# Optimization experiments

Hardware: AMD Instinct MI355X
Metric: run time of the kernel (lower is better)

The kernel has to match this reference:

```python
import jax, jax.numpy as jnp
import numpy as np

BN_EPS = 1e-5
NN_EPS = 1e-8

def _bn_relu(h, gamma, beta):
    # training-mode BatchNorm1d over (B, L) per channel, biased variance
    mean = jnp.mean(h, axis=(0, 2), keepdims=True)
    var = jnp.mean((h - mean) ** 2, axis=(0, 2), keepdims=True)
    hn = (h - mean) * jax.lax.rsqrt(var + BN_EPS)
    return jax.nn.relu(hn * gamma[None, :, None] + beta[None, :, None])

def setup_inputs() -> dict:
    key = jax.random.key(0)
    ks = jax.random.split(key, 8)
    B, N, M, Cin, Cout = 2, 2048, 8192, 512, 256
    return {
        "x1": jax.random.normal(ks[0], (B, N, Cin), jnp.float32),
        "p1": jax.random.uniform(ks[1], (B, N, 3), jnp.float32),
        "x2": jax.random.normal(ks[2], (B, M, Cout), jnp.float32),
        "p2": jax.random.uniform(ks[3], (B, M, 3), jnp.float32),
        "W_up": jax.random.normal(ks[4], (Cout, Cin), jnp.float32) * (1.0 / np.sqrt(Cin)),
        "gamma_up": jnp.ones((Cout,), jnp.float32),
        "beta_up": jnp.zeros((Cout,), jnp.float32),
        "W_lat": jax.random.normal(ks[5], (Cout, Cout), jnp.float32) * (1.0 / np.sqrt(Cout)),
        "gamma_lat": jnp.ones((Cout,), jnp.float32),
        "beta_lat": jnp.zeros((Cout,), jnp.float32),
    }

def reference(x1, p1, x2, p2, W_up, gamma_up, beta_up, W_lat, gamma_lat, beta_lat):
    B, M, _ = p2.shape
    # up_mlp: 1x1 conv (bias=False) + BN + ReLU -> (B, Cout, N)
    h1 = _bn_relu(jnp.einsum('bnc,oc->bon', x1, W_up), gamma_up, beta_up)
    # three_nn: squared distances from each p2 query to all p1 points
    d2 = (jnp.sum(p2 ** 2, -1)[:, :, None] + jnp.sum(p1 ** 2, -1)[:, None, :]
          - 2.0 * jnp.einsum('bmd,bnd->bmn', p2, p1))  # (B, M, N)
    neg_d, idx = jax.lax.top_k(-d2, 3)                 # 3 smallest squared dists
    dist = -neg_d                                      # (B, M, 3)
    dist_recip = 1.0 / (dist + NN_EPS)
    weight = dist_recip / jnp.sum(dist_recip, axis=2, keepdims=True)  # (B, M, 3)
    # three_interpolate: weighted gather of h1 along point axis
    C = h1.shape[1]
    g = jnp.take_along_axis(h1, idx.reshape(B, 1, M * 3), axis=2).reshape(B, C, M, 3)
    interp = jnp.einsum('bcmk,bmk->bcm', g, weight)    # (B, Cout, M)
    # lateral_mlp on x2
    h2 = _bn_relu(jnp.einsum('bmc,oc->bom', x2, W_lat), gamma_lat, beta_lat)
    y = interp + h2                                    # (B, Cout, M)
    return jnp.transpose(y, (0, 2, 1)), p2             # (B, M, Cout), (B, M, 3)
```

## Files before the change

### kernel.cpp

```cpp
#include <hip/hip_runtime.h>

#define BATCH 2
#define NPTS  2048
#define MPTS  8192
#define CIN1  512
#define CIN2  256
#define COUT  256
#define ROWS1 (BATCH*NPTS)
#define ROWS2 (BATCH*MPTS)
#define BN_EPS 1e-5f
#define NN_EPS 1e-8f

#define NCHUNK 16
#define CHUNK  (NPTS / NCHUNK)

typedef __attribute__((ext_vector_type(8))) short  bf16x8;
typedef __attribute__((ext_vector_type(4))) float  f32x4;

#define AS1 __attribute__((address_space(1)))
#define AS3 __attribute__((address_space(3)))

__device__ __forceinline__ unsigned short bf16_rne(float x) {
    unsigned u = __float_as_uint(x);
    u += 0x7FFFu + ((u >> 16) & 1u);
    return (unsigned short)(u >> 16);
}
__device__ __forceinline__ float bf16_f32(unsigned short h) {
    return __uint_as_float(((unsigned)h) << 16);
}

__device__ __forceinline__ void gload16(const void* g, void* l) {
    __builtin_amdgcn_global_load_lds((const AS1 unsigned int*)g,
                                     (AS3 unsigned int*)l, 16, 0, 0);
}

__global__ __launch_bounds__(256)
void split_pre(const float* __restrict__ x1, const float* __restrict__ x2,
               const float* __restrict__ wu, const float* __restrict__ wl,
               unsigned short* __restrict__ x1h, unsigned short* __restrict__ x1l,
               unsigned short* __restrict__ x2h, unsigned short* __restrict__ x2l,
               unsigned short* __restrict__ wuh, unsigned short* __restrict__ wul,
               unsigned short* __restrict__ wlh, unsigned short* __restrict__ wll) {
    const int bid = blockIdx.x;
    const float* src; unsigned short *dh, *dl; int K, tile;
    if (bid < 1024)      { src = x1; dh = x1h; dl = x1l; K = CIN1; tile = bid; }
    else if (bid < 3072) { src = x2; dh = x2h; dl = x2l; K = CIN2; tile = bid - 1024; }
    else if (bid < 3136) { src = wu; dh = wuh; dl = wul; K = CIN1; tile = bid - 3072; }
    else                 { src = wl; dh = wlh; dl = wll; K = CIN2; tile = bid - 3136; }
    const int ktiles = K / 32;
    const int rt = tile / ktiles, kt = tile - rt * ktiles;
    const int t = threadIdx.x, row = t >> 2, lg = t & 3;

    const float* s = src + (size_t)(rt * 64 + row) * K + kt * 32 + lg * 8;
    const float4 v0 = *(const float4*)s;
    const float4 v1 = *(const float4*)(s + 4);
    const float vv[8] = {v0.x, v0.y, v0.z, v0.w, v1.x, v1.y, v1.z, v1.w};
    bf16x8 h, l;
    #pragma unroll
    for (int i = 0; i < 8; ++i) {
        const unsigned short hh = bf16_rne(vv[i]);
        h[i] = (short)hh;
        l[i] = (short)bf16_rne(vv[i] - bf16_f32(hh));
    }
    const unsigned off = ((unsigned)(row * 64 + lg * 16)) ^ ((unsigned)((row & 7) << 4));
    *(bf16x8*)((char*)dh + (size_t)tile * 4096 + off) = h;
    *(bf16x8*)((char*)dl + (size_t)tile * 4096 + off) = l;
}

template<int KTILES, int KSPLIT, bool FUSE_STATS>
__global__ __launch_bounds__(256)
void gemm_pre(const unsigned short* __restrict__ Ah_img, const unsigned short* __restrict__ Al_img,
              const unsigned short* __restrict__ Bh_img, const unsigned short* __restrict__ Bl_img,
              float* __restrict__ C, float* __restrict__ stats) {
    constexpr int KT = KTILES / KSPLIT;
    __shared__ __align__(16) unsigned char lds[2][4][4096];
    __shared__ float red[64][8];

    const int tid = threadIdx.x;
    const int lane = tid & 63, wid = tid >> 6;
    const int m0 = blockIdx.y * 64, o0 = blockIdx.x * 64;
    const int kt0 = blockIdx.z * KT;
    const int wy = wid >> 1, wx = wid & 1;
    const int lr = lane & 15, lg = lane >> 4;

    const unsigned short* src;
    size_t base;
    switch (wid) {
        case 0:  src = Ah_img; base = ((size_t)blockIdx.y * KTILES + kt0) * 2048; break;
        case 1:  src = Al_img; base = ((size_t)blockIdx.y * KTILES + kt0) * 2048; break;
        case 2:  src = Bh_img; base = ((size_t)blockIdx.x * KTILES + kt0) * 2048; break;
        default: src = Bl_img; base = ((size_t)blockIdx.x * KTILES + kt0) * 2048; break;
    }

    f32x4 acc[2][2];
    #pragma unroll
    for (int i = 0; i < 2; ++i)
        #pragma unroll
        for (int j = 0; j < 2; ++j)
            acc[i][j] = (f32x4){0.f, 0.f, 0.f, 0.f};

    auto STAGE = [&](int buf, int t) {
        const unsigned short* s = src + base + (size_t)t * 2048;
        char* l = (char*)&lds[buf][wid][0];
        #pragma unroll
        for (int c = 0; c < 4; ++c)
            gload16(s + c * 512 + lane * 8, l + c * 1024);
    };

    auto FOFF = [&](int row) -> int {
        return (row * 64 + lg * 16) ^ ((row & 7) << 4);
    };

    STAGE(0, 0);
    asm volatile("s_waitcnt vmcnt(0)" ::: "memory");
    __builtin_amdgcn_s_barrier();
    __builtin_amdgcn_sched_barrier(0);

    int cur = 0;
    for (int t = 0; t < KT; ++t) {
        if (t + 1 < KT) STAGE(cur ^ 1, t + 1);

        const char* LAh = (const char*)&lds[cur][0][0];
        const char* LAl = (const char*)&lds[cur][1][0];
        const char* LBh = (const char*)&lds[cur][2][0];
        const char* LBl = (const char*)&lds[cur][3][0];

        bf16x8 fah[2], fal[2], fbh[2], fbl[2];
        #pragma unroll
        for (int i = 0; i < 2; ++i) {
            const int off = FOFF(wy * 32 + i * 16 + lr);
            fah[i] = *(const bf16x8*)(LAh + off);
            fal[i] = *(const bf16x8*)(LAl + off);
        }
        #pragma unroll
        for (int j = 0; j < 2; ++j) {
            const int off = FOFF(wx * 32 + j * 16 + lr);
            fbh[j] = *(const bf16x8*)(LBh + off);
            fbl[j] = *(const bf16x8*)(LBl + off);
        }
        #pragma unroll
        for (int i = 0; i < 2; ++i)
            #pragma unroll
            for (int j = 0; j < 2; ++j) {
                acc[i][j] = __builtin_amdgcn_mfma_f32_16x16x32_bf16(fah[i], fbh[j], acc[i][j], 0, 0, 0);
                acc[i][j] = __builtin_amdgcn_mfma_f32_16x16x32_bf16(fal[i], fbh[j], acc[i][j], 0, 0, 0);
                acc[i][j] = __builtin_amdgcn_mfma_f32_16x16x32_bf16(fah[i], fbl[j], acc[i][j], 0, 0, 0);
            }

        asm volatile("s_waitcnt vmcnt(0)" ::: "memory");
        __builtin_amdgcn_s_barrier();
        __builtin_amdgcn_sched_barrier(0);
        cur ^= 1;
    }

    #pragma unroll
    for (int i = 0; i < 2; ++i)
        #pragma unroll
        for (int j = 0; j < 2; ++j) {
            const int col = o0 + wx * 32 + j * 16 + lr;
            const int rbase = m0 + wy * 32 + i * 16 + lg * 4;
            #pragma unroll
            for (int r = 0; r < 4; ++r) {
                if (KSPLIT > 1)
                    atomicAdd(&C[(size_t)(rbase + r) * COUT + col], acc[i][j][r]);
                else
                    C[(size_t)(rbase + r) * COUT + col] = acc[i][j][r];
            }
        }

    if constexpr (FUSE_STATS) {
        #pragma unroll
        for (int j = 0; j < 2; ++j) {
            float s = 0.f;
            #pragma unroll
            for (int i = 0; i < 2; ++i)
                #pragma unroll
                for (int r = 0; r < 4; ++r)
                    s += acc[i][j][r];
            red[wx * 32 + j * 16 + lr][wy * 4 + lg] = s;
        }
        __syncthreads();
        if (tid < 64) {
            float s = 0.f;
            #pragma unroll
            for (int k = 0; k < 8; ++k) s += red[tid][k];
            atomicAdd(&stats[o0 + tid], s);
        }
        __syncthreads();
        #pragma unroll
        for (int j = 0; j < 2; ++j) {
            float q = 0.f;
            #pragma unroll
            for (int i = 0; i < 2; ++i)
                #pragma unroll
                for (int r = 0; r < 4; ++r)
                    q = fmaf(acc[i][j][r], acc[i][j][r], q);
            red[wx * 32 + j * 16 + lr][wy * 4 + lg] = q;
        }
        __syncthreads();
        if (tid < 64) {
            float q = 0.f;
            #pragma unroll
            for (int k = 0; k < 8; ++k) q += red[tid][k];
            atomicAdd(&stats[COUT + o0 + tid], q);
        }
    }
}

__global__ __launch_bounds__(256)
void colsum256(const float* __restrict__ X, int rowsPerBlock,
               float* __restrict__ out) {
    const int c = threadIdx.x;
    const int r0 = blockIdx.x * rowsPerBlock;
    float s = 0.f, q = 0.f;
    for (int r = 0; r < rowsPerBlock; ++r) {
        float v = X[(size_t)(r0 + r) * COUT + c];
        s += v;
        q = fmaf(v, v, q);
    }
    atomicAdd(&out[c], s);
    atomicAdd(&out[COUT + c], q);
}

__global__ __launch_bounds__(256)
void three_nn_part(const float* __restrict__ p1, const float* __restrict__ p2,
                   float2* __restrict__ part) {
    __shared__ float4 pts[CHUNK];
    const int b = blockIdx.z;
    const int c = blockIdx.y;
    const int t = threadIdx.x;
    const int n0 = c * CHUNK;
    if (t < CHUNK) {
        const float* P1 = p1 + ((size_t)b * NPTS + n0) * 3;
        float x = P1[t * 3 + 0], y = P1[t * 3 + 1], z = P1[t * 3 + 2];
        pts[t] = make_float4(x, y, z, x * x + y * y + z * z);
    }
    __syncthreads();
    const int m = blockIdx.x * 256 + t;
    const float* q = p2 + ((size_t)b * MPTS + m) * 3;
    const float qx = q[0], qy = q[1], qz = q[2];
    const float s2 = qx * qx + qy * qy + qz * qz;
    float d0 = 1e30f, d1 = 1e30f, d2 = 1e30f;
    int   i0 = 0,     i1 = 0,     i2 = 0;
    #pragma unroll 4
    for (int n = 0; n < CHUNK; ++n) {
        float4 p = pts[n];
        float dot = p.x * qx + p.y * qy + p.z * qz;
        float d = s2 + p.w - 2.0f * dot;
        if (d < d2) {
            if (d < d1) {
                d2 = d1; i2 = i1;
                if (d < d0) { d1 = d0; i1 = i0; d0 = d; i0 = n0 + n; }
                else        { d1 = d;  i1 = n0 + n; }
            } else { d2 = d; i2 = n0 + n; }
        }
    }
    float2* o = part + ((size_t)(b * MPTS + m) * NCHUNK + c) * 3;
    o[0] = make_float2(d0, __int_as_float(i0));
    o[1] = make_float2(d1, __int_as_float(i1));
    o[2] = make_float2(d2, __int_as_float(i2));
}

__global__ __launch_bounds__(256)
void final_combine(const float* __restrict__ h1, const float* __restrict__ stats,
                   const float* __restrict__ g1, const float* __restrict__ b1,
                   const float* __restrict__ g2, const float* __restrict__ b2,
                   const float2* __restrict__ part, float* __restrict__ out) {
    const int t = threadIdx.x;
    const int row = blockIdx.x * 4 + (t >> 6);
    const int c = (t & 63) * 4;
    const int b = row >> 13;

    float d0 = 1e30f, d1 = 1e30f, d2 = 1e30f;
    int   i0 = 0,     i1 = 0,     i2 = 0;
    {
        const float4* pp = (const float4*)(part + (size_t)row * NCHUNK * 3);
        #pragma unroll
        for (int j = 0; j < NCHUNK * 3 / 2; ++j) {
            float4 v = pp[j];
            #pragma unroll
            for (int h = 0; h < 2; ++h) {
                float d = h ? v.z : v.x;
                int   i = __float_as_int(h ? v.w : v.y);
                if (d < d2) {
                    if (d < d1) {
                        d2 = d1; i2 = i1;
                        if (d < d0) { d1 = d0; i1 = i0; d0 = d; i0 = i; }
                        else        { d1 = d;  i1 = i; }
                    } else { d2 = d; i2 = i; }
                }
            }
        }
    }
    const float r0 = 1.0f / (d0 + NN_EPS);
    const float r1 = 1.0f / (d1 + NN_EPS);
    const float r2 = 1.0f / (d2 + NN_EPS);
    const float irs = 1.0f / (r0 + r1 + r2);
    const float w0 = r0 * irs, w1 = r1 * irs, w2 = r2 * irs;

    const float4 sum1 = *(const float4*)&stats[c];
    const float4 sq1  = *(const float4*)&stats[COUT + c];
    const float4 sum2 = *(const float4*)&stats[512 + c];
    const float4 sq2  = *(const float4*)&stats[768 + c];
    const float4 gg1  = *(const float4*)&g1[c];
    const float4 bb1  = *(const float4*)&b1[c];
    const float4 gg2  = *(const float4*)&g2[c];
    const float4 bb2  = *(const float4*)&b2[c];

    const float inv1 = 1.0f / (float)ROWS1, inv2 = 1.0f / (float)ROWS2;
    float4 sc1, sh1, sc2, sh2;
    {
        float m, v;
        m = sum1.x*inv1; v = fmaf(-m,m,sq1.x*inv1); sc1.x = gg1.x/sqrtf(v+BN_EPS); sh1.x = fmaf(-m,sc1.x,bb1.x);
        m = sum1.y*inv1; v = fmaf(-m,m,sq1.y*inv1); sc1.y = gg1.y/sqrtf(v+BN_EPS); sh1.y = fmaf(-m,sc1.y,bb1.y);
        m = sum1.z*inv1; v = fmaf(-m,m,sq1.z*inv1); sc1.z = gg1.z/sqrtf(v+BN_EPS); sh1.z = fmaf(-m,sc1.z,bb1.z);
        m = sum1.w*inv1; v = fmaf(-m,m,sq1.w*inv1); sc1.w = gg1.w/sqrtf(v+BN_EPS); sh1.w = fmaf(-m,sc1.w,bb1.w);
        m = sum2.x*inv2; v = fmaf(-m,m,sq2.x*inv2); sc2.x = gg2.x/sqrtf(v+BN_EPS); sh2.x = fmaf(-m,sc2.x,bb2.x);
        m = sum2.y*inv2; v = fmaf(-m,m,sq2.y*inv2); sc2.y = gg2.y/sqrtf(v+BN_EPS); sh2.y = fmaf(-m,sc2.y,bb2.y);
        m = sum2.z*inv2; v = fmaf(-m,m,sq2.z*inv2); sc2.z = gg2.z/sqrtf(v+BN_EPS); sh2.z = fmaf(-m,sc2.z,bb2.z);
        m = sum2.w*inv2; v = fmaf(-m,m,sq2.w*inv2); sc2.w = gg2.w/sqrtf(v+BN_EPS); sh2.w = fmaf(-m,sc2.w,bb2.w);
    }

    const float* hb = h1 + (size_t)b * NPTS * COUT + c;
    const float4 h0 = *(const float4*)(hb + (size_t)i0 * COUT);
    const float4 h4 = *(const float4*)(hb + (size_t)i1 * COUT);
    const float4 h8 = *(const float4*)(hb + (size_t)i2 * COUT);

    const size_t oi = (size_t)row * COUT + c;
    float4 yv = *(const float4*)&out[oi];
    float4 r;
    r.x = fmaxf(fmaf(yv.x, sc2.x, sh2.x), 0.f)
        + w0 * fmaxf(fmaf(h0.x, sc1.x, sh1.x), 0.f)
        + w1 * fmaxf(fmaf(h4.x, sc1.x, sh1.x), 0.f)
        + w2 * fmaxf(fmaf(h8.x, sc1.x, sh1.x), 0.f);
    r.y = fmaxf(fmaf(yv.y, sc2.y, sh2.y), 0.f)
        + w0 * fmaxf(fmaf(h0.y, sc1.y, sh1.y), 0.f)
        + w1 * fmaxf(fmaf(h4.y, sc1.y, sh1.y), 0.f)
        + w2 * fmaxf(fmaf(h8.y, sc1.y, sh1.y), 0.f);
    r.z = fmaxf(fmaf(yv.z, sc2.z, sh2.z), 0.f)
        + w0 * fmaxf(fmaf(h0.z, sc1.z, sh1.z), 0.f)
        + w1 * fmaxf(fmaf(h4.z, sc1.z, sh1.z), 0.f)
        + w2 * fmaxf(fmaf(h8.z, sc1.z, sh1.z), 0.f);
    r.w = fmaxf(fmaf(yv.w, sc2.w, sh2.w), 0.f)
        + w0 * fmaxf(fmaf(h0.w, sc1.w, sh1.w), 0.f)
        + w1 * fmaxf(fmaf(h4.w, sc1.w, sh1.w), 0.f)
        + w2 * fmaxf(fmaf(h8.w, sc1.w, sh1.w), 0.f);
    *(float4*)&out[oi] = r;
}

extern "C" void kernel_launch(void* const* d_in, const int* in_sizes, int n_in,
                              void* d_out, int out_size, void* d_ws, size_t ws_size,
                              hipStream_t stream) {
    const float* x1       = (const float*)d_in[0];
    const float* p1       = (const float*)d_in[1];
    const float* x2       = (const float*)d_in[2];
    const float* p2       = (const float*)d_in[3];
    const float* W_up     = (const float*)d_in[4];
    const float* gamma_up = (const float*)d_in[5];
    const float* beta_up  = (const float*)d_in[6];
    const float* W_lat    = (const float*)d_in[7];
    const float* gamma_lat= (const float*)d_in[8];
    const float* beta_lat = (const float*)d_in[9];
    float* out = (float*)d_out;

    char* w = (char*)d_ws;
    unsigned short* x1h = (unsigned short*)(w);
    unsigned short* x1l = (unsigned short*)(w + (4u<<20));
    unsigned short* x2h = (unsigned short*)(w + (8u<<20));
    unsigned short* x2l = (unsigned short*)(w + (16u<<20));
    unsigned short* wuh = (unsigned short*)(w + (24u<<20));
    unsigned short* wul = (unsigned short*)(w + (24u<<20) + (256u<<10));
    unsigned short* wlh = (unsigned short*)(w + (24u<<20) + (512u<<10));
    unsigned short* wll = (unsigned short*)(w + (24u<<20) + (640u<<10));
    float*  h1    = (float*)(w + (25u<<20));
    float*  stats = (float*)(w + (29u<<20));
    float2* part  = (float2*)(w + (29u<<20) + (16u<<10));

    hipMemsetAsync(stats, 0, 1024 * sizeof(float), stream);
    hipMemsetAsync(h1, 0, (size_t)ROWS1 * COUT * sizeof(float), stream);

    split_pre<<<3168, 256, 0, stream>>>(x1, x2, W_up, W_lat,
                                        x1h, x1l, x2h, x2l, wuh, wul, wlh, wll);

    gemm_pre<CIN1/32, 4, false><<<dim3(COUT/64, ROWS1/64, 4), 256, 0, stream>>>(
        x1h, x1l, wuh, wul, h1, nullptr);
    colsum256<<<256, 256, 0, stream>>>(h1, ROWS1 / 256, stats);

    gemm_pre<CIN2/32, 1, true><<<dim3(COUT/64, ROWS2/64, 1), 256, 0, stream>>>(
        x2h, x2l, wlh, wll, out, stats + 512);

    three_nn_part<<<dim3(MPTS / 256, NCHUNK, BATCH), 256, 0, stream>>>(p1, p2, part);

    final_combine<<<ROWS2 / 4, 256, 0, stream>>>(h1, stats, gamma_up, beta_up,
                                                 gamma_lat, beta_lat, part, out);

    hipMemcpyAsync(out + (size_t)ROWS2 * COUT, p2,
                   (size_t)ROWS2 * 3 * sizeof(float),
                   hipMemcpyDeviceToDevice, stream);
}
```

Baseline: 194.7 us.

## Merge prep with three_nn, merge both GEMMs, triple-buffer LDS pipeline

The bf16 split preprocessing and the three-NN partial search now share one launch, with block-index ranges selecting the work. Both projection GEMMs are merged into a single launch so the two independent workloads fill the GPU together. The GEMM K-loop moves from double to triple buffering with a partial vmcnt wait, so loads stay two stages ahead. The two memsets become one contiguous memset covering h1 and stats. This cuts launch count and tail idle time, but raises LDS per block, which may lower occupancy.

Result: no change. 192.2 us (-1.3%).

```diff
diff --git a/kernel.cpp b/kernel.cpp
--- a/kernel.cpp
+++ b/kernel.cpp
@@ -28,68 +28,111 @@
 __device__ __forceinline__ float bf16_f32(unsigned short h) {
     return __uint_as_float(((unsigned)h) << 16);
 }
-
 __device__ __forceinline__ void gload16(const void* g, void* l) {
     __builtin_amdgcn_global_load_lds((const AS1 unsigned int*)g,
                                      (AS3 unsigned int*)l, 16, 0, 0);
 }
 
 __global__ __launch_bounds__(256)
-void split_pre(const float* __restrict__ x1, const float* __restrict__ x2,
-               const float* __restrict__ wu, const float* __restrict__ wl,
-               unsigned short* __restrict__ x1h, unsigned short* __restrict__ x1l,
-               unsigned short* __restrict__ x2h, unsigned short* __restrict__ x2l,
-               unsigned short* __restrict__ wuh, unsigned short* __restrict__ wul,
-               unsigned short* __restrict__ wlh, unsigned short* __restrict__ wll) {
+void prep_fused(const float* __restrict__ x1, const float* __restrict__ x2,
+                const float* __restrict__ wu, const float* __restrict__ wl,
+                const float* __restrict__ p1, const float* __restrict__ p2,
+                unsigned short* __restrict__ x1h, unsigned short* __restrict__ x1l,
+                unsigned short* __restrict__ x2h, unsigned short* __restrict__ x2l,
+                unsigned short* __restrict__ wuh, unsigned short* __restrict__ wul,
+                unsigned short* __restrict__ wlh, unsigned short* __restrict__ wll,
+                float2* __restrict__ part) {
     const int bid = blockIdx.x;
-    const float* src; unsigned short *dh, *dl; int K, tile;
-    if (bid < 1024)      { src = x1; dh = x1h; dl = x1l; K = CIN1; tile = bid; }
-    else if (bid < 3072) { src = x2; dh = x2h; dl = x2l; K = CIN2; tile = bid - 1024; }
-    else if (bid < 3136) { src = wu; dh = wuh; dl = wul; K = CIN1; tile = bid - 3072; }
-    else                 { src = wl; dh = wlh; dl = wll; K = CIN2; tile = bid - 3136; }
-    const int ktiles = K / 32;
-    const int rt = tile / ktiles, kt = tile - rt * ktiles;
-    const int t = threadIdx.x, row = t >> 2, lg = t & 3;
-
-    const float* s = src + (size_t)(rt * 64 + row) * K + kt * 32 + lg * 8;
-    const float4 v0 = *(const float4*)s;
-    const float4 v1 = *(const float4*)(s + 4);
-    const float vv[8] = {v0.x, v0.y, v0.z, v0.w, v1.x, v1.y, v1.z, v1.w};
-    bf16x8 h, l;
-    #pragma unroll
-    for (int i = 0; i < 8; ++i) {
-        const unsigned short hh = bf16_rne(vv[i]);
-        h[i] = (short)hh;
-        l[i] = (short)bf16_rne(vv[i] - bf16_f32(hh));
-    }
-    const unsigned off = ((unsigned)(row * 64 + lg * 16)) ^ ((unsigned)((row & 7) << 4));
-    *(bf16x8*)((char*)dh + (size_t)tile * 4096 + off) = h;
-    *(bf16x8*)((char*)dl + (size_t)tile * 4096 + off) = l;
-}
+    const int t = threadIdx.x;
+    if (bid < 3168) {
+        const float* src; unsigned short *dh, *dl; int K, tile;
+        if (bid < 1024)      { src = x1; dh = x1h; dl = x1l; K = CIN1; tile = bid; }
+        else if (bid < 3072) { src = x2; dh = x2h; dl = x2l; K = CIN2; tile = bid - 1024; }
+        else if (bid < 3136) { src = wu; dh = wuh; dl = wul; K = CIN1; tile = bid - 3072; }
+        else                 { src = wl; dh = wlh; dl = wll; K = CIN2; tile = bid - 3136; }
+        const int ktiles = K / 32;
+        const int rt = tile / ktiles, kt = tile - rt * ktiles;
+        const int row = t >> 2, lg = t & 3;
+        const float* s = src + (size_t)(rt * 64 + row) * K + kt * 32 + lg * 8;
+        const float4 v0 = *(const float4*)s;
+        const float4 v1 = *(const float4*)(s + 4);
+        const float vv[8] = {v0.x, v0.y, v0.z, v0.w, v1.x, v1.y, v1.z, v1.w};
+        bf16x8 h, l;
+        #pragma unroll
+        for (int i = 0; i < 8; ++i) {
+            const unsigned short hh = bf16_rne(vv[i]);
+            h[i] = (short)hh;
+            l[i] = (short)bf16_rne(vv[i] - bf16_f32(hh));
+        }
+        const unsigned off = ((unsigned)(row * 64 + lg * 16)) ^ ((unsigned)((row & 7) << 4));
+        *(bf16x8*)((char*)dh + (size_t)tile * 4096 + off) = h;
+        *(bf16x8*)((char*)dl + (size_t)tile * 4096 + off) = l;
+    } else {
+        __shared__ float4 pts[CHUNK];
+        const int q = bid - 3168;
+        const int b = q >> 9;
+        const int r = q & 511;
+        const int ck = r >> 5;
+        const int mblk = r & 31;
+        const int n0 = ck * CHUNK;
+        if (t < CHUNK) {
+            const float* P1 = p1 + ((size_t)b * NPTS + n0) * 3;
+            float x = P1[t * 3 + 0], y = P1[t * 3 + 1], z = P1[t * 3 + 2];
+            pts[t] = make_float4(x, y, z, x * x + y * y + z * z);
+        }
+        __syncthreads();
+        const int m = mblk * 256 + t;
+        const float* qp = p2 + ((size_t)b * MPTS + m) * 3;
+        const float qx = qp[0], qy = qp[1], qz = qp[2];
+        const float s2 = qx * qx + qy * qy + qz * qz;
+        float d0 = 1e30f, d1 = 1e30f, d2 = 1e30f;
+        int   i0 = 0,     i1 = 0,     i2 = 0;
+        #pragma unroll 4
+        for (int n = 0; n < CHUNK; ++n) {
+            float4 p = pts[n];
+            float dot = p.x * qx + p.y * qy + p.z * qz;
+            float d = s2 + p.w - 2.0f * dot;
+            if (d < d2) {
+                if (d < d1) {
+                    d2 = d1; i2 = i1;
+                    if (d < d0) { d1 = d0; i1 = i0; d0 = d; i0 = n0 + n; }
+                    else        { d1 = d;  i1 = n0 + n; }
+                } else { d2 = d; i2 = n0 + n; }
+            }
+        }
+        float2* o = part + ((size_t)(b * MPTS + m) * NCHUNK + ck) * 3;
+        o[0] = make_float2(d0, __int_as_float(i0));
+        o[1] = make_float2(d1, __int_as_float(i1));
+        o[2] = make_float2(d2, __int_as_float(i2));
+    }
+}
+
+struct GemmLds {
+    unsigned char buf[3][4][4096];
+    float red[64][8];
+};
 
 template<int KTILES, int KSPLIT, bool FUSE_STATS>
-__global__ __launch_bounds__(256)
-void gemm_pre(const unsigned short* __restrict__ Ah_img, const unsigned short* __restrict__ Al_img,
-              const unsigned short* __restrict__ Bh_img, const unsigned short* __restrict__ Bl_img,
-              float* __restrict__ C, float* __restrict__ stats) {
+__device__ __forceinline__ void gemm_body(
+        const unsigned short* __restrict__ Ah_img, const unsigned short* __restrict__ Al_img,
+        const unsigned short* __restrict__ Bh_img, const unsigned short* __restrict__ Bl_img,
+        float* __restrict__ C, float* __restrict__ stats,
+        int bx, int by, int bz, GemmLds& S) {
     constexpr int KT = KTILES / KSPLIT;
-    __shared__ __align__(16) unsigned char lds[2][4][4096];
-    __shared__ float red[64][8];
-
     const int tid = threadIdx.x;
     const int lane = tid & 63, wid = tid >> 6;
-    const int m0 = blockIdx.y * 64, o0 = blockIdx.x * 64;
-    const int kt0 = blockIdx.z * KT;
+    const int m0 = by * 64, o0 = bx * 64;
+    const int kt0 = bz * KT;
     const int wy = wid >> 1, wx = wid & 1;
     const int lr = lane & 15, lg = lane >> 4;
 
     const unsigned short* src;
     size_t base;
     switch (wid) {
-        case 0:  src = Ah_img; base = ((size_t)blockIdx.y * KTILES + kt0) * 2048; break;
-        case 1:  src = Al_img; base = ((size_t)blockIdx.y * KTILES + kt0) * 2048; break;
-        case 2:  src = Bh_img; base = ((size_t)blockIdx.x * KTILES + kt0) * 2048; break;
-        default: src = Bl_img; base = ((size_t)blockIdx.x * KTILES + kt0) * 2048; break;
+        case 0:  src = Ah_img; base = ((size_t)by * KTILES + kt0) * 2048; break;
+        case 1:  src = Al_img; base = ((size_t)by * KTILES + kt0) * 2048; break;
+        case 2:  src = Bh_img; base = ((size_t)bx * KTILES + kt0) * 2048; break;
+        default: src = Bl_img; base = ((size_t)bx * KTILES + kt0) * 2048; break;
     }
 
     f32x4 acc[2][2];
@@ -99,31 +142,32 @@
         for (int j = 0; j < 2; ++j)
             acc[i][j] = (f32x4){0.f, 0.f, 0.f, 0.f};
 
-    auto STAGE = [&](int buf, int t) {
-        const unsigned short* s = src + base + (size_t)t * 2048;
-        char* l = (char*)&lds[buf][wid][0];
+    auto STAGE = [&](int buf, int tt) {
+        const unsigned short* s = src + base + (size_t)tt * 2048;
+        char* l = (char*)&S.buf[buf][wid][0];
         #pragma unroll
         for (int c = 0; c < 4; ++c)
-            gload16(s + c * 512 + lane * 8, l + c * 1024);
+            gload16(s + c * 512 + (size_t)lane * 8, l + c * 1024);
     };
-
     auto FOFF = [&](int row) -> int {
         return (row * 64 + lg * 16) ^ ((row & 7) << 4);
     };
 
     STAGE(0, 0);
-    asm volatile("s_waitcnt vmcnt(0)" ::: "memory");
-    __builtin_amdgcn_s_barrier();
-    __builtin_amdgcn_sched_barrier(0);
-
-    int cur = 0;
+    if (KT > 1) STAGE(1, 1);
+
     for (int t = 0; t < KT; ++t) {
-        if (t + 1 < KT) STAGE(cur ^ 1, t + 1);
-
-        const char* LAh = (const char*)&lds[cur][0][0];
-        const char* LAl = (const char*)&lds[cur][1][0];
-        const char* LBh = (const char*)&lds[cur][2][0];
-        const char* LBl = (const char*)&lds[cur][3][0];
+        if (t + 1 < KT) asm volatile("s_waitcnt vmcnt(4)" ::: "memory");
+        else            asm volatile("s_waitcnt vmcnt(0)" ::: "memory");
+        __builtin_amdgcn_s_barrier();
+        __builtin_amdgcn_sched_barrier(0);
+        if (t + 2 < KT) STAGE((t + 2) % 3, t + 2);
+
+        const int cb = t % 3;
+        const char* LAh = (const char*)&S.buf[cb][0][0];
+        const char* LAl = (const char*)&S.buf[cb][1][0];
+        const char* LBh = (const char*)&S.buf[cb][2][0];
+        const char* LBl = (const char*)&S.buf[cb][3][0];
 
         bf16x8 fah[2], fal[2], fbh[2], fbl[2];
         #pragma unroll
@@ -146,11 +190,6 @@
                 acc[i][j] = __builtin_amdgcn_mfma_f32_16x16x32_bf16(fal[i], fbh[j], acc[i][j], 0, 0, 0);
                 acc[i][j] = __builtin_amdgcn_mfma_f32_16x16x32_bf16(fah[i], fbl[j], acc[i][j], 0, 0, 0);
             }
-
-        asm volatile("s_waitcnt vmcnt(0)" ::: "memory");
-        __builtin_amdgcn_s_barrier();
-        __builtin_amdgcn_sched_barrier(0);
-        cur ^= 1;
     }
 
     #pragma unroll
@@ -177,13 +216,13 @@
                 #pragma unroll
                 for (int r = 0; r < 4; ++r)
                     s += acc[i][j][r];
-            red[wx * 32 + j * 16 + lr][wy * 4 + lg] = s;
+            S.red[wx * 32 + j * 16 + lr][wy * 4 + lg] = s;
         }
         __syncthreads();
         if (tid < 64) {
             float s = 0.f;
             #pragma unroll
-            for (int k = 0; k < 8; ++k) s += red[tid][k];
+            for (int k = 0; k < 8; ++k) s += S.red[tid][k];
             atomicAdd(&stats[o0 + tid], s);
         }
         __syncthreads();
@@ -195,15 +234,33 @@
                 #pragma unroll
                 for (int r = 0; r < 4; ++r)
                     q = fmaf(acc[i][j][r], acc[i][j][r], q);
-            red[wx * 32 + j * 16 + lr][wy * 4 + lg] = q;
+            S.red[wx * 32 + j * 16 + lr][wy * 4 + lg] = q;
         }
         __syncthreads();
         if (tid < 64) {
             float q = 0.f;
             #pragma unroll
-            for (int k = 0; k < 8; ++k) q += red[tid][k];
+            for (int k = 0; k < 8; ++k) q += S.red[tid][k];
             atomicAdd(&stats[COUT + o0 + tid], q);
         }
+    }
+}
+
+__global__ __launch_bounds__(256)
+void gemm_fused(const unsigned short* __restrict__ x1h, const unsigned short* __restrict__ x1l,
+                const unsigned short* __restrict__ wuh, const unsigned short* __restrict__ wul,
+                const unsigned short* __restrict__ x2h, const unsigned short* __restrict__ x2l,
+                const unsigned short* __restrict__ wlh, const unsigned short* __restrict__ wll,
+                float* __restrict__ h1, float* __restrict__ out, float* __restrict__ stats) {
+    __shared__ GemmLds S;
+    const int bid = blockIdx.x;
+    if (bid < 1024) {
+        gemm_body<CIN2/32, 1, true>(x2h, x2l, wlh, wll, out, stats + 512,
+                                    bid & 3, bid >> 2, 0, S);
+    } else {
+        const int q = bid - 1024;
+        gemm_body<CIN1/32, 4, false>(x1h, x1l, wuh, wul, h1, nullptr,
+                                     q & 3, (q & 255) >> 2, q >> 8, S);
     }
 }
 
@@ -220,45 +277,6 @@
     }
     atomicAdd(&out[c], s);
     atomicAdd(&out[COUT + c], q);
-}
-
-__global__ __launch_bounds__(256)
-void three_nn_part(const float* __restrict__ p1, const float* __restrict__ p2,
-                   float2* __restrict__ part) {
-    __shared__ float4 pts[CHUNK];
-    const int b = blockIdx.z;
-    const int c = blockIdx.y;
-    const int t = threadIdx.x;
-    const int n0 = c * CHUNK;
-    if (t < CHUNK) {
-        const float* P1 = p1 + ((size_t)b * NPTS + n0) * 3;
-        float x = P1[t * 3 + 0], y = P1[t * 3 + 1], z = P1[t * 3 + 2];
-        pts[t] = make_float4(x, y, z, x * x + y * y + z * z);
-    }
-    __syncthreads();
-    const int m = blockIdx.x * 256 + t;
-    const float* q = p2 + ((size_t)b * MPTS + m) * 3;
-    const float qx = q[0], qy = q[1], qz = q[2];
-    const float s2 = qx * qx + qy * qy + qz * qz;
-    float d0 = 1e30f, d1 = 1e30f, d2 = 1e30f;
-    int   i0 = 0,     i1 = 0,     i2 = 0;
-    #pragma unroll 4
-    for (int n = 0; n < CHUNK; ++n) {
-        float4 p = pts[n];
-        float dot = p.x * qx + p.y * qy + p.z * qz;
-        float d = s2 + p.w - 2.0f * dot;
-        if (d < d2) {
-            if (d < d1) {
-                d2 = d1; i2 = i1;
-                if (d < d0) { d1 = d0; i1 = i0; d0 = d; i0 = n0 + n; }
-                else        { d1 = d;  i1 = n0 + n; }
-            } else { d2 = d; i2 = n0 + n; }
-        }
-    }
-    float2* o = part + ((size_t)(b * MPTS + m) * NCHUNK + c) * 3;
-    o[0] = make_float2(d0, __int_as_float(i0));
-    o[1] = make_float2(d1, __int_as_float(i1));
-    o[2] = make_float2(d2, __int_as_float(i2));
 }
 
 __global__ __launch_bounds__(256)
@@ -376,20 +394,16 @@
     float*  stats = (float*)(w + (29u<<20));
     float2* part  = (float2*)(w + (29u<<20) + (16u<<10));
 
-    hipMemsetAsync(stats, 0, 1024 * sizeof(float), stream);
-    hipMemsetAsync(h1, 0, (size_t)ROWS1 * COUT * sizeof(float), stream);
-
-    split_pre<<<3168, 256, 0, stream>>>(x1, x2, W_up, W_lat,
-                                        x1h, x1l, x2h, x2l, wuh, wul, wlh, wll);
-
-    gemm_pre<CIN1/32, 4, false><<<dim3(COUT/64, ROWS1/64, 4), 256, 0, stream>>>(
-        x1h, x1l, wuh, wul, h1, nullptr);
+    hipMemsetAsync(h1, 0, (4u << 20) + 4096, stream);
+
+    prep_fused<<<3168 + 1024, 256, 0, stream>>>(x1, x2, W_up, W_lat, p1, p2,
+                                                x1h, x1l, x2h, x2l,
+                                                wuh, wul, wlh, wll, part);
+
+    gemm_fused<<<2048, 256, 0, stream>>>(x1h, x1l, wuh, wul,
+                                         x2h, x2l, wlh, wll, h1, out, stats);
+
     colsum256<<<256, 256, 0, stream>>>(h1, ROWS1 / 256, stats);
-
-    gemm_pre<CIN2/32, 1, true><<<dim3(COUT/64, ROWS2/64, 1), 256, 0, stream>>>(
-        x2h, x2l, wlh, wll, out, stats + 512);
-
-    three_nn_part<<<dim3(MPTS / 256, NCHUNK, BATCH), 256, 0, stream>>>(p1, p2, part);
 
     final_combine<<<ROWS2 / 4, 256, 0, stream>>>(h1, stats, gamma_up, beta_up,
                                                  gamma_lat, beta_lat, part, out);
```
